# Performance work log

Hardware: AMD Instinct MI355X
Metric: run time of the kernel (lower is better)

## Reference

```python
import jax, jax.numpy as jnp
import numpy as np

# Config (DiffWave-style)
C = 64        # channels
K = 3         # kernel_size
L = 30        # num_layers
CYCLES = 3    # num_cycles
DRATE = 2     # dilation_rate
ITER = 50     # diffusion steps
ESIZE = 128   # embedding_size
EPROJ = 512   # embedding_proj
EFACT = 4.0   # embedding_factor
B, T = 4, 16384
LAYERS_PER_CYCLE = L // CYCLES
DILATIONS = [DRATE ** (i % LAYERS_PER_CYCLE) for i in range(L)]
INV_SQRT2 = 1.0 / np.sqrt(2.0).astype(np.float32)


def _embed_table():
    # [ITER, ESIZE] sinusoidal noise-schedule embedding (deterministic buffer)
    logit = jnp.linspace(0.0, 1.0, ESIZE // 2)
    exp = jnp.power(10.0, logit * EFACT)
    t = jnp.arange(1, ITER + 1, dtype=jnp.float32)
    comp = exp[None, :] * t[:, None]
    return jnp.concatenate([jnp.sin(comp), jnp.cos(comp)], axis=-1)


def _dconv(x, w, d):
    # x: [B,T,Cin], w: [K,Cin,Cout], SAME padding, dilation d -> [B,T,Cout]
    return jax.lax.conv_general_dilated(
        x, w, window_strides=(1,), padding='SAME', rhs_dilation=(d,),
        dimension_numbers=('NWC', 'WIO', 'NWC'))


def setup_inputs() -> dict:
    key = jax.random.key(0)
    ks = jax.random.split(key, 20)
    g = lambda k, shape, fan_in: (jax.random.normal(k, shape) / np.sqrt(fan_in)).astype(jnp.float32)
    return {
        'signal': jax.random.normal(ks[0], (B, T), dtype=jnp.float32),
        'timestep': jax.random.randint(ks[1], (B,), 1, ITER + 1, dtype=jnp.int32),
        'in_w': g(ks[2], (1, C), 1),
        'in_b': jnp.zeros((C,), jnp.float32),
        'pe0_w': g(ks[3], (ESIZE, EPROJ), ESIZE),
        'pe0_b': jnp.zeros((EPROJ,), jnp.float32),
        'pe1_w': g(ks[4], (EPROJ, EPROJ), EPROJ),
        'pe1_b': jnp.zeros((EPROJ,), jnp.float32),
        'blk_emb_w': g(ks[5], (L, EPROJ, C), EPROJ),
        'blk_emb_b': jnp.zeros((L, C), jnp.float32),
        'blk_conv_w': g(ks[6], (L, K, C, 2 * C), K * C),
        'blk_conv_b': jnp.zeros((L, 2 * C), jnp.float32),
        'blk_res_w': g(ks[7], (L - 1, C, C), C),
        'blk_res_b': jnp.zeros((L - 1, C), jnp.float32),
        'blk_skip_w': g(ks[8], (L, C, C), C),
        'blk_skip_b': jnp.zeros((L, C), jnp.float32),
        'out0_w': g(ks[9], (C, C), C),
        'out0_b': jnp.zeros((C,), jnp.float32),
        'out1_w': g(ks[10], (C, 1), C),
        'out1_b': jnp.zeros((1,), jnp.float32),
    }


def reference(signal, timestep, in_w, in_b, pe0_w, pe0_b, pe1_w, pe1_b,
              blk_emb_w, blk_emb_b, blk_conv_w, blk_conv_b,
              blk_res_w, blk_res_b, blk_skip_w, blk_skip_b,
              out0_w, out0_b, out1_w, out1_b):
    # input 1x1 conv + relu: [B,T] -> [B,T,C]
    x = jax.nn.relu(signal[..., None] * in_w[0][None, None, :] + in_b)
    # noise-schedule embedding [B,ESIZE] -> swish MLP -> [B,EPROJ]
    embed = _embed_table()[timestep - 1]
    embed = jax.nn.swish(embed @ pe0_w + pe0_b)
    embed = jax.nn.swish(embed @ pe1_w + pe1_b)
    skip_sum = jnp.zeros_like(x)
    for i in range(L):
        e = embed @ blk_emb_w[i] + blk_emb_b[i]           # [B,C]
        h = x + e[:, None, :]                              # [B,T,C]
        y = _dconv(h, blk_conv_w[i], DILATIONS[i]) + blk_conv_b[i]  # [B,T,2C]
        z = jnp.tanh(y[..., :C]) * jax.nn.sigmoid(y[..., C:])       # gated
        if i < L - 1:
            x = (z @ blk_res_w[i] + blk_res_b[i] + x) * INV_SQRT2
        skip_sum = skip_sum + (z @ blk_skip_w[i] + blk_skip_b[i])
    ctx = skip_sum / np.sqrt(L).astype(np.float32)
    ctx = jax.nn.relu(ctx @ out0_w + out0_b)
    out = ctx @ out1_w + out1_b                            # [B,T,1]
    return jnp.squeeze(out, axis=-1)
```

## Files before the change

kernel.cpp:

```cpp
#include <hip/hip_runtime.h>
#include <math.h>

#define TT 16384
#define BB 4
#define CC 64
#define LL 30

typedef _Float16 f16;
typedef _Float16 f16x4 __attribute__((ext_vector_type(4)));
typedef _Float16 f16x8 __attribute__((ext_vector_type(8)));
typedef float f32x4 __attribute__((ext_vector_type(4)));
typedef unsigned int u32;

#define MFMA(a, b, c) __builtin_amdgcn_mfma_f32_16x16x32_f16(a, b, c, 0, 0, 0)

__device__ __forceinline__ float fsig(float x) { return 1.0f / (1.0f + __expf(-x)); }
__device__ __forceinline__ float ftanhf(float x) { return 1.0f - 2.0f / (__expf(2.0f * x) + 1.0f); }

__device__ __forceinline__ void gl_lds16(const void* g, void* l) {
    __builtin_amdgcn_global_load_lds((const __attribute__((address_space(1))) u32*)g,
                                     (__attribute__((address_space(3))) u32*)l, 16, 0, 0);
}

__global__ void pack_weights(const float* __restrict__ conv_w, const float* __restrict__ res_w,
                             const float* __restrict__ skip_w, const float* __restrict__ out0_w,
                             f16* __restrict__ wcv, f16* __restrict__ wrs, f16* __restrict__ wsk,
                             f16* __restrict__ wo0) {
    const int total_c = LL * 6 * 8 * 64 * 8;
    const int total_r = (LL - 1) * 2 * 4 * 64 * 8;
    const int total_s = LL * 2 * 4 * 64 * 8;
    const int total_o = 2 * 4 * 64 * 8;
    const int total = total_c + total_r + total_s + total_o;
    for (int i = blockIdx.x * blockDim.x + threadIdx.x; i < total; i += gridDim.x * blockDim.x) {
        if (i < total_c) {
            int e = i & 7, lane = (i >> 3) & 63, mf = (i >> 9) & 7, rest = i >> 12;
            int ks = rest % 6, l = rest / 6;
            int cin = (ks & 1) * 32 + (lane >> 4) * 8 + e;
            int tap = ks >> 1;
            int cout = mf * 16 + (lane & 15);
            wcv[i] = (f16)conv_w[(((size_t)l * 3 + tap) * 64 + cin) * 128 + cout];
        } else if (i < total_c + total_r) {
            int j = i - total_c;
            int e = j & 7, lane = (j >> 3) & 63, mf = (j >> 9) & 3, kk = (j >> 11) & 1, l = j >> 12;
            int cin = kk * 32 + (lane >> 4) * 8 + e;
            int cout = mf * 16 + (lane & 15);
            wrs[j] = (f16)res_w[((size_t)l * 64 + cin) * 64 + cout];
        } else if (i < total_c + total_r + total_s) {
            int j = i - total_c - total_r;
            int e = j & 7, lane = (j >> 3) & 63, mf = (j >> 9) & 3, kk = (j >> 11) & 1, l = j >> 12;
            int cin = kk * 32 + (lane >> 4) * 8 + e;
            int cout = mf * 16 + (lane & 15);
            wsk[j] = (f16)skip_w[((size_t)l * 64 + cin) * 64 + cout];
        } else {
            int j = i - total_c - total_r - total_s;
            int e = j & 7, lane = (j >> 3) & 63, mf = (j >> 9) & 3, kk = (j >> 11) & 1;
            int cin = kk * 32 + (lane >> 4) * 8 + e;
            int c = mf * 16 + (lane & 15);
            wo0[j] = (f16)out0_w[cin * 64 + c];
        }
    }
}

__global__ void init_x_kernel(const float* __restrict__ signal, const float* __restrict__ in_w,
                              const float* __restrict__ in_b, f16* __restrict__ x0) {
    int i = blockIdx.x * 256 + threadIdx.x;
    int bt = i >> 3, g = i & 7;
    float s = signal[bt];
    f32x4 w0 = *(const f32x4*)&in_w[g * 8];
    f32x4 w1 = *(const f32x4*)&in_w[g * 8 + 4];
    f32x4 b0 = *(const f32x4*)&in_b[g * 8];
    f32x4 b1 = *(const f32x4*)&in_b[g * 8 + 4];
    f16x8 o;
#pragma unroll
    for (int j = 0; j < 4; ++j) {
        o[j] = (f16)fmaxf(s * w0[j] + b0[j], 0.f);
        o[4 + j] = (f16)fmaxf(s * w1[j] + b1[j], 0.f);
    }
    *(f16x8*)&x0[(size_t)bt * CC + g * 8] = o;
}

__global__ void embed_stage1(const int* __restrict__ timestep, const float* __restrict__ pe0_w,
                             const float* __restrict__ pe0_b, float* __restrict__ h1) {
    __shared__ float emb[BB * 128];
    const int tid = threadIdx.x;
    for (int i = tid; i < BB * 128; i += 256) {
        int b = i >> 7, j = i & 127, jj = j & 63;
        float logit = (jj == 63) ? 1.0f : (float)jj * (1.0f / 63.0f);
        double e10 = pow(10.0, (double)(4.0f * logit));
        float comp = (float)e10 * (float)timestep[b];
        emb[i] = (j < 64) ? (float)sin((double)comp) : (float)cos((double)comp);
    }
    __syncthreads();
    const int col = blockIdx.x * 64 + (tid & 63), b = tid >> 6;
    float s = 0.f;
    for (int j = 0; j < 128; ++j) s += emb[b * 128 + j] * pe0_w[j * 512 + col];
    s += pe0_b[col];
    h1[b * 512 + col] = s * fsig(s);
}

__global__ void embed_stage2(const float* __restrict__ h1, const float* __restrict__ pe1_w,
                             const float* __restrict__ pe1_b, float* __restrict__ embed2) {
    __shared__ float hs[BB * 512];
    const int tid = threadIdx.x;
    for (int i = tid; i < BB * 512; i += 256) hs[i] = h1[i];
    __syncthreads();
    const int col = blockIdx.x * 64 + (tid & 63), b = tid >> 6;
    float s = 0.f;
    for (int j = 0; j < 512; ++j) s += hs[b * 512 + j] * pe1_w[j * 512 + col];
    s += pe1_b[col];
    embed2[b * 512 + col] = s * fsig(s);
}

__global__ void e_kernel(const float* __restrict__ embed2, const float* __restrict__ blk_emb_w,
                         const float* __restrict__ blk_emb_b, float* __restrict__ e_out) {
    const int l = blockIdx.x, b = blockIdx.y;
    const int tid = threadIdx.x;
    __shared__ float em[512];
    __shared__ float red[256];
    for (int i = tid; i < 512; i += 256) em[i] = embed2[b * 512 + i];
    __syncthreads();
    const int c = tid & 63, part = tid >> 6;
    float s0 = 0.f, s1 = 0.f;
    for (int j = part * 128; j < part * 128 + 128; j += 2) {
        s0 += em[j] * blk_emb_w[((size_t)l * 512 + j) * 64 + c];
        s1 += em[j + 1] * blk_emb_w[((size_t)l * 512 + j + 1) * 64 + c];
    }
    red[tid] = s0 + s1;
    __syncthreads();
    if (tid < 64)
        e_out[(l * BB + b) * 64 + tid] =
            red[tid] + red[tid + 64] + red[tid + 128] + red[tid + 192] + blk_emb_b[l * 64 + tid];
}

__global__ void evec2_kernel(const float* __restrict__ e_in, const float* __restrict__ conv_w,
                             const float* __restrict__ conv_b, float* __restrict__ evec) {
    const int l = blockIdx.x, tap = blockIdx.y, b = blockIdx.z;
    const int n = threadIdx.x;
    __shared__ float es[64];
    if (n < 64) es[n] = e_in[(l * BB + b) * 64 + n];
    __syncthreads();
    const float* cw = conv_w + ((size_t)(l * 3 + tap) * 64) * 128;
    float a0 = 0.f, a1 = 0.f, a2 = 0.f, a3 = 0.f;
#pragma unroll
    for (int k = 0; k < 64; k += 4) {
        a0 += es[k] * cw[k * 128 + n];
        a1 += es[k + 1] * cw[(k + 1) * 128 + n];
        a2 += es[k + 2] * cw[(k + 2) * 128 + n];
        a3 += es[k + 3] * cw[(k + 3) * 128 + n];
    }
    float s = a0 + a1 + a2 + a3 + ((tap == 1) ? conv_b[l * 128 + n] : 0.f);
    evec[((size_t)(l * 4 + b) * 3 + tap) * 128 + n] = s;
}

__global__ void sbsum_kernel(const float* __restrict__ skip_b, float* __restrict__ sbsum) {
    int c = threadIdx.x;
    float s = 0.f;
    for (int l = 0; l < LL; ++l) s += skip_b[l * 64 + c];
    sbsum[c] = s;
}

__launch_bounds__(256)
__global__ void layer_kernel(const f16* __restrict__ xin, f16* __restrict__ xout,
                             f16* __restrict__ zg,
                             const f16* __restrict__ wcv,
                             const f16* __restrict__ wrs,
                             const float* __restrict__ evec_l,
                             const float* __restrict__ res_b,
                             const f16* __restrict__ zpage, int d) {
    __shared__ f16 xs[3 * 64 * 64];
    __shared__ f16 zs[64 * 64];
    const int tid = threadIdx.x, lane = tid & 63, w = tid >> 6;
    const int lrow = lane & 15, lk = lane >> 4;
    const int b = blockIdx.y, t0 = blockIdx.x * 64;
    const f16* xb = xin + (size_t)b * TT * CC;
    f16* zb = zg + (size_t)b * TT * CC;

#pragma unroll
    for (int j = 0; j < 6; ++j) {
        int chunk = j * 4 + w;
        int gid = chunk * 64 + lane;
        int tap = gid >> 9, row = (gid >> 3) & 63, g = gid & 7;
        int t = t0 + row + (tap - 1) * d;
        const f16* src = ((unsigned)t < TT) ? (xb + (size_t)t * CC + ((g ^ (row & 7)) << 3)) : zpage;
        gl_lds16(src, (void*)((char*)xs + chunk * 1024));
    }
    __syncthreads();

    f32x4 acc[2][4] = {};
#pragma unroll
    for (int ks = 0; ks < 6; ++ks) {
        const int tap = ks >> 1, kk = ks & 1;
        f16x8 aw0 = *(const f16x8*)&wcv[((ks * 8 + w) * 64 + lane) * 8];
        f16x8 aw1 = *(const f16x8*)&wcv[((ks * 8 + w + 4) * 64 + lane) * 8];
#pragma unroll
        for (int nfi = 0; nfi < 4; ++nfi) {
            int trow = nfi * 16 + lrow;
            int r = tap * 64 + trow;
            int g = kk * 4 + lk;
            f16x8 bx = *(const f16x8*)&xs[r * 64 + ((g ^ (r & 7)) << 3)];
            acc[0][nfi] = MFMA(aw0, bx, acc[0][nfi]);
            acc[1][nfi] = MFMA(aw1, bx, acc[1][nfi]);
        }
    }

    const float* evb = evec_l + b * 384;
    const int ca = w * 16 + lk * 4;
    const int gz = ca >> 3;
    f32x4 e0a = *(const f32x4*)&evb[ca], e1a = *(const f32x4*)&evb[128 + ca],
          e2a = *(const f32x4*)&evb[256 + ca];
    f32x4 e0b = *(const f32x4*)&evb[64 + ca], e1b = *(const f32x4*)&evb[192 + ca],
          e2b = *(const f32x4*)&evb[320 + ca];
#pragma unroll
    for (int nfi = 0; nfi < 4; ++nfi) {
        int trow = nfi * 16 + lrow;
        int t = t0 + trow;
        float m0 = (t >= d) ? 1.f : 0.f;
        float m2 = (t + d < TT) ? 1.f : 0.f;
        f16x4 zo;
#pragma unroll
        for (int r = 0; r < 4; ++r) {
            float ya = acc[0][nfi][r] + e1a[r] + m0 * e0a[r] + m2 * e2a[r];
            float yb = acc[1][nfi][r] + e1b[r] + m0 * e0b[r] + m2 * e2b[r];
            zo[r] = (f16)(ftanhf(ya) * fsig(yb));
        }
        *(f16x4*)&zs[trow * 64 + ((gz ^ (trow & 7)) << 3) + (ca & 7)] = zo;
        *(f16x4*)&zb[(size_t)(t0 + trow) * CC + ca] = zo;
    }

    if (wrs != nullptr) {
        __syncthreads();
        f32x4 accR[4] = {};
#pragma unroll
        for (int kk = 0; kk < 2; ++kk) {
            f16x8 ar_ = *(const f16x8*)&wrs[((kk * 4 + w) * 64 + lane) * 8];
#pragma unroll
            for (int nfi = 0; nfi < 4; ++nfi) {
                int trow = nfi * 16 + lrow;
                int g = kk * 4 + lk;
                f16x8 bz = *(const f16x8*)&zs[trow * 64 + ((g ^ (trow & 7)) << 3)];
                accR[nfi] = MFMA(ar_, bz, accR[nfi]);
            }
        }
        f16* xob = xout + (size_t)b * TT * CC;
        f32x4 rb4 = *(const f32x4*)&res_b[ca];
#pragma unroll
        for (int nfi = 0; nfi < 4; ++nfi) {
            int trow = nfi * 16 + lrow;
            int rr = 64 + trow;
            f16x4 xv = *(const f16x4*)&xs[rr * 64 + ((gz ^ (rr & 7)) << 3) + (ca & 7)];
            f16x4 xo;
#pragma unroll
            for (int r = 0; r < 4; ++r)
                xo[r] = (f16)((accR[nfi][r] + rb4[r] + (float)xv[r]) * 0.70710678118654752f);
            *(f16x4*)&xob[(size_t)(t0 + trow) * CC + ca] = xo;
        }
    }
}

__launch_bounds__(256)
__global__ void skip_head(const f16* __restrict__ zbuf, const f16* __restrict__ z29,
                          const f16* __restrict__ wsk, const f16* __restrict__ wo0,
                          const float* __restrict__ sbsum, const float* __restrict__ out0_b,
                          const float* __restrict__ out1_w, const float* __restrict__ out1_b,
                          float* __restrict__ out) {
    __shared__ f16 zb[4][64 * 64];
    const int tid = threadIdx.x, lane = tid & 63, w = tid >> 6;
    const int lrow = lane & 15, lk = lane >> 4;
    const int lin = blockIdx.x;
    const int lin2 = (lin & 7) * 128 + (lin >> 3);
    const int b = lin2 >> 8, tile = lin2 & 255;
    const int t0 = tile * 64;
    const int trow = w * 16 + lrow;

#define STAGE_Z(L, BUF)                                                                       \
    {                                                                                         \
        const f16* zl =                                                                       \
            (((L) < LL - 1) ? (zbuf + (size_t)(L)*BB * TT * CC) : z29) + (size_t)b * TT * CC; \
        _Pragma("unroll") for (int j = 0; j < 2; ++j) {                                       \
            int chunk = j * 4 + w;                                                            \
            int gid = chunk * 64 + lane;                                                      \
            int r = gid >> 3, g = gid & 7;                                                    \
            gl_lds16(zl + (size_t)(t0 + r) * CC + ((g ^ (r & 7)) << 3),                       \
                     (void*)((char*)zb[BUF] + chunk * 1024));                                 \
        }                                                                                     \
    }

    f32x4 accS[4] = {};
    STAGE_Z(0, 0);
    STAGE_Z(1, 1);
    for (int l = 0; l < LL; ++l) {
        if (l + 2 < LL) STAGE_Z(l + 2, (l + 2) & 3);
        if (l < LL - 2) {
            asm volatile("s_waitcnt vmcnt(4)" ::: "memory");
        } else if (l == LL - 2) {
            asm volatile("s_waitcnt vmcnt(2)" ::: "memory");
        } else {
            asm volatile("s_waitcnt vmcnt(0)" ::: "memory");
        }
        __builtin_amdgcn_s_barrier();
        __builtin_amdgcn_sched_barrier(0);
        const f16* wl = wsk + (size_t)l * 4096;
        const f16* zcur = zb[l & 3];
#pragma unroll
        for (int kk = 0; kk < 2; ++kk) {
            int g = kk * 4 + lk;
            f16x8 bz = *(const f16x8*)&zcur[trow * 64 + ((g ^ (trow & 7)) << 3)];
#pragma unroll
            for (int mf = 0; mf < 4; ++mf) {
                f16x8 as_ = *(const f16x8*)&wl[((kk * 4 + mf) * 64 + lane) * 8];
                accS[mf] = MFMA(as_, bz, accS[mf]);
            }
        }
    }

    __syncthreads();
    const float invL = 0.18257418583505537f;
#pragma unroll
    for (int mf = 0; mf < 4; ++mf) {
        const int ca = mf * 16 + lk * 4;
        f32x4 sb4 = *(const f32x4*)&sbsum[ca];
        const int g = ca >> 3;
        f16x4 sn;
#pragma unroll
        for (int r = 0; r < 4; ++r) sn[r] = (f16)((accS[mf][r] + sb4[r]) * invL);
        *(f16x4*)&zb[0][trow * 64 + ((g ^ (trow & 7)) << 3) + (ca & 7)] = sn;
    }
    __syncthreads();
    f32x4 accO[4] = {};
#pragma unroll
    for (int kk = 0; kk < 2; ++kk) {
        int g = kk * 4 + lk;
        f16x8 bz = *(const f16x8*)&zb[0][trow * 64 + ((g ^ (trow & 7)) << 3)];
#pragma unroll
        for (int mf = 0; mf < 4; ++mf) {
            f16x8 aw = *(const f16x8*)&wo0[((kk * 4 + mf) * 64 + lane) * 8];
            accO[mf] = MFMA(aw, bz, accO[mf]);
        }
    }
    float pv = 0.f;
    const float b1 = out1_b[0];
#pragma unroll
    for (int mf = 0; mf < 4; ++mf) {
        int c = mf * 16 + lk * 4;
        f32x4 b0 = *(const f32x4*)&out0_b[c];
        f32x4 w1 = *(const f32x4*)&out1_w[c];
#pragma unroll
        for (int r = 0; r < 4; ++r) pv += fmaxf(accO[mf][r] + b0[r], 0.f) * w1[r];
    }
    pv += __shfl_xor(pv, 16);
    pv += __shfl_xor(pv, 32);
    if (lane < 16) out[(size_t)b * TT + t0 + w * 16 + lane] = pv + b1;
#undef STAGE_Z
}

extern "C" void kernel_launch(void* const* d_in, const int* in_sizes, int n_in,
                              void* d_out, int out_size, void* d_ws, size_t ws_size,
                              hipStream_t stream) {
    const float* signal = (const float*)d_in[0];
    const int* timestep = (const int*)d_in[1];
    const float* in_w = (const float*)d_in[2];
    const float* in_b = (const float*)d_in[3];
    const float* pe0_w = (const float*)d_in[4];
    const float* pe0_b = (const float*)d_in[5];
    const float* pe1_w = (const float*)d_in[6];
    const float* pe1_b = (const float*)d_in[7];
    const float* blk_emb_w = (const float*)d_in[8];
    const float* blk_emb_b = (const float*)d_in[9];
    const float* blk_conv_w = (const float*)d_in[10];
    const float* blk_conv_b = (const float*)d_in[11];
    const float* blk_res_w = (const float*)d_in[12];
    const float* blk_res_b = (const float*)d_in[13];
    const float* blk_skip_w = (const float*)d_in[14];
    const float* blk_skip_b = (const float*)d_in[15];
    const float* out0_w = (const float*)d_in[16];
    const float* out0_b = (const float*)d_in[17];
    const float* out1_w = (const float*)d_in[18];
    const float* out1_b = (const float*)d_in[19];

    char* p = (char*)d_ws;
    const size_t xhsz = (size_t)BB * TT * CC * sizeof(f16);
    f16* xa = (f16*)p; p += xhsz;
    f16* xb2 = (f16*)p; p += xhsz;
    f16* wcv = (f16*)p; p += (size_t)737280 * 2;
    f16* wrs = (f16*)p; p += (size_t)118784 * 2;
    f16* wsk = (f16*)p; p += (size_t)122880 * 2;
    f16* wo0 = (f16*)p; p += (size_t)4096 * 2;
    float* h1 = (float*)p; p += 4 * 512 * sizeof(float);
    float* embed2 = (float*)p; p += 4 * 512 * sizeof(float);
    float* e_buf = (float*)p; p += (size_t)LL * BB * 64 * sizeof(float);
    float* evec = (float*)p; p += (size_t)LL * 4 * 3 * 128 * sizeof(float);
    float* sbsum = (float*)p; p += 64 * sizeof(float);
    f16* zpage = (f16*)p; p += 256;
    p = (char*)(((size_t)p + 255) & ~(size_t)255);
    f16* zbuf = (f16*)p; p += (size_t)(LL - 1) * xhsz;

    hipMemsetAsync(zpage, 0, 256, stream);
    pack_weights<<<1024, 256, 0, stream>>>(blk_conv_w, blk_res_w, blk_skip_w, out0_w,
                                           wcv, wrs, wsk, wo0);
    init_x_kernel<<<2048, 256, 0, stream>>>(signal, in_w, in_b, xa);
    embed_stage1<<<8, 256, 0, stream>>>(timestep, pe0_w, pe0_b, h1);
    embed_stage2<<<8, 256, 0, stream>>>(h1, pe1_w, pe1_b, embed2);
    e_kernel<<<dim3(LL, BB), 256, 0, stream>>>(embed2, blk_emb_w, blk_emb_b, e_buf);
    evec2_kernel<<<dim3(LL, 3, BB), 128, 0, stream>>>(e_buf, blk_conv_w, blk_conv_b, evec);
    sbsum_kernel<<<1, 64, 0, stream>>>(blk_skip_b, sbsum);

    f16* cur = xa;
    f16* nxt = xb2;
    for (int i = 0; i < LL; ++i) {
        int d = 1 << (i % 10);
        bool last = (i == LL - 1);
        f16* zg = last ? xa : (zbuf + (size_t)i * BB * TT * CC);
        layer_kernel<<<dim3(TT / 64, BB), 256, 0, stream>>>(
            cur, nxt, zg,
            wcv + (size_t)i * 24576,
            last ? nullptr : (wrs + (size_t)i * 4096),
            evec + (size_t)i * 1536,
            last ? nullptr : (blk_res_b + i * 64),
            zpage, d);
        if (!last) { f16* t = cur; cur = nxt; nxt = t; }
    }

    skip_head<<<(BB * TT) / 64, 256, 0, stream>>>(zbuf, xa, wsk, wo0, sbsum, out0_b, out1_w,
                                                  out1_b, (float*)d_out);
}
```

Before: 567.6 us.

## Fuse first four dilated layers of each cycle into one LDS-resident kernel

Adds a group kernel that runs layers with dilations 1,2,4,8 back to back on a 128-step tile plus a 32-step halo on each side, keeping the residual stream in double-buffered LDS. It replaces four separate layer launches per cycle, each of which round-trips x through global memory. The cost is redundant halo computation (192 rows computed for 128 useful), clamped reads at the halo edges, and more LDS per block, which may lower occupancy. The final z buffer pointer is adjusted so the last layer's gate output lands in the right buffer for the skip head.

```diff
diff --git a/kernel.cpp b/kernel.cpp
--- a/kernel.cpp
+++ b/kernel.cpp
@@ -160,12 +160,122 @@
 }
 
 __launch_bounds__(256)
+__global__ void group4_kernel(const f16* __restrict__ xin, f16* __restrict__ xout,
+                              f16* __restrict__ zg_base,
+                              const f16* __restrict__ wcv_g,
+                              const f16* __restrict__ wrs_g,
+                              const float* __restrict__ evec_g,
+                              const float* __restrict__ res_b_g,
+                              const f16* __restrict__ zpage) {
+    __shared__ f16 lds[2 * 192 * 64];
+    const int tid = threadIdx.x, lane = tid & 63, w = tid >> 6;
+    const int lrow = lane & 15, lk = lane >> 4;
+    const int b = blockIdx.y, t0 = blockIdx.x * 128;
+    const int ca = w * 16 + lk * 4, gz = ca >> 3;
+    const f16* xbg = xin + (size_t)b * TT * CC;
+
+#pragma unroll
+    for (int j = 0; j < 6; ++j) {
+        int chunk = j * 4 + w;
+        int gid = chunk * 64 + lane;
+        int r = gid >> 3, g = gid & 7;
+        int t = t0 - 32 + r;
+        const f16* src = ((unsigned)t < TT) ? (xbg + (size_t)t * CC + ((g ^ (r & 7)) << 3)) : zpage;
+        gl_lds16(src, (void*)((char*)lds + chunk * 1024));
+    }
+    __syncthreads();
+
+#pragma unroll
+    for (int li = 0; li < 4; ++li) {
+        const int d = 1 << li;
+        f16* xc = lds + (li & 1) * (192 * 64);
+        f16* xn = lds + ((li & 1) ^ 1) * (192 * 64);
+        const f16* wcv_l = wcv_g + (size_t)li * 24576;
+        const f16* wrs_l = wrs_g + (size_t)li * 4096;
+        f16* zb_g = zg_base + (size_t)li * ((size_t)BB * TT * CC) + (size_t)b * TT * CC;
+        const float* evb = evec_g + li * 1536 + b * 384;
+
+        f32x4 acc0[12] = {}, acc1[12] = {};
+#pragma unroll
+        for (int ks = 0; ks < 6; ++ks) {
+            const int tap = ks >> 1, kk = ks & 1;
+            f16x8 aw0 = *(const f16x8*)&wcv_l[((ks * 8 + w) * 64 + lane) * 8];
+            f16x8 aw1 = *(const f16x8*)&wcv_l[((ks * 8 + w + 4) * 64 + lane) * 8];
+#pragma unroll
+            for (int nt = 0; nt < 12; ++nt) {
+                int rr = nt * 16 + lrow + (tap - 1) * d;
+                rr = (rr < 0) ? 0 : (rr > 191 ? 191 : rr);
+                int g = kk * 4 + lk;
+                f16x8 bx = *(const f16x8*)&xc[rr * 64 + ((g ^ (rr & 7)) << 3)];
+                acc0[nt] = MFMA(aw0, bx, acc0[nt]);
+                acc1[nt] = MFMA(aw1, bx, acc1[nt]);
+            }
+        }
+        __syncthreads();
+
+        f32x4 e0a = *(const f32x4*)&evb[ca], e1a = *(const f32x4*)&evb[128 + ca],
+              e2a = *(const f32x4*)&evb[256 + ca];
+        f32x4 e0b = *(const f32x4*)&evb[64 + ca], e1b = *(const f32x4*)&evb[192 + ca],
+              e2b = *(const f32x4*)&evb[320 + ca];
+        f16x4 xv[12];
+#pragma unroll
+        for (int nt = 0; nt < 12; ++nt) {
+            int lr = nt * 16 + lrow;
+            int t = t0 - 32 + lr;
+            xv[nt] = *(const f16x4*)&xc[lr * 64 + ((gz ^ (lr & 7)) << 3) + (ca & 7)];
+            float m0 = (t >= d) ? 1.f : 0.f;
+            float m2 = (t + d < TT) ? 1.f : 0.f;
+            f16x4 zo;
+#pragma unroll
+            for (int r = 0; r < 4; ++r) {
+                float ya = acc0[nt][r] + e1a[r] + m0 * e0a[r] + m2 * e2a[r];
+                float yb = acc1[nt][r] + e1b[r] + m0 * e0b[r] + m2 * e2b[r];
+                zo[r] = (f16)(ftanhf(ya) * fsig(yb));
+            }
+            *(f16x4*)&xc[lr * 64 + ((gz ^ (lr & 7)) << 3) + (ca & 7)] = zo;
+            if (nt >= 2 && nt < 10) *(f16x4*)&zb_g[(size_t)t * CC + ca] = zo;
+        }
+        __syncthreads();
+
+        f32x4 accR[12] = {};
+#pragma unroll
+        for (int kk = 0; kk < 2; ++kk) {
+            f16x8 ar = *(const f16x8*)&wrs_l[((kk * 4 + w) * 64 + lane) * 8];
+#pragma unroll
+            for (int nt = 0; nt < 12; ++nt) {
+                int lr = nt * 16 + lrow;
+                int g = kk * 4 + lk;
+                f16x8 bz = *(const f16x8*)&xc[lr * 64 + ((g ^ (lr & 7)) << 3)];
+                accR[nt] = MFMA(ar, bz, accR[nt]);
+            }
+        }
+        f32x4 rb4 = *(const f32x4*)&res_b_g[li * 64 + ca];
+        f16* xog = xout + (size_t)b * TT * CC;
+#pragma unroll
+        for (int nt = 0; nt < 12; ++nt) {
+            int lr = nt * 16 + lrow;
+            int t = t0 - 32 + lr;
+            bool tin = ((unsigned)t < TT);
+            f16x4 xo;
+#pragma unroll
+            for (int r = 0; r < 4; ++r)
+                xo[r] = tin ? (f16)((accR[nt][r] + rb4[r] + (float)xv[nt][r]) * 0.70710678118654752f)
+                            : (f16)0;
+            if (li < 3) {
+                *(f16x4*)&xn[lr * 64 + ((gz ^ (lr & 7)) << 3) + (ca & 7)] = xo;
+            } else if (nt >= 2 && nt < 10) {
+                *(f16x4*)&xog[(size_t)t * CC + ca] = xo;
+            }
+        }
+        __syncthreads();
+    }
+}
+
+__launch_bounds__(256)
 __global__ void layer_kernel(const f16* __restrict__ xin, f16* __restrict__ xout,
                              f16* __restrict__ zg,
-                             const f16* __restrict__ wcv,
-                             const f16* __restrict__ wrs,
-                             const float* __restrict__ evec_l,
-                             const float* __restrict__ res_b,
+                             const f16* __restrict__ wcv, const f16* __restrict__ wrs,
+                             const float* __restrict__ evec_l, const float* __restrict__ res_b,
                              const f16* __restrict__ zpage, int d) {
     __shared__ f16 xs[3 * 64 * 64];
     __shared__ f16 zs[64 * 64];
@@ -379,6 +489,7 @@
 
     char* p = (char*)d_ws;
     const size_t xhsz = (size_t)BB * TT * CC * sizeof(f16);
+    const size_t BTC = (size_t)BB * TT * CC;
     f16* xa = (f16*)p; p += xhsz;
     f16* xb2 = (f16*)p; p += xhsz;
     f16* wcv = (f16*)p; p += (size_t)737280 * 2;
@@ -406,20 +517,28 @@
 
     f16* cur = xa;
     f16* nxt = xb2;
-    for (int i = 0; i < LL; ++i) {
-        int d = 1 << (i % 10);
-        bool last = (i == LL - 1);
-        f16* zg = last ? xa : (zbuf + (size_t)i * BB * TT * CC);
-        layer_kernel<<<dim3(TT / 64, BB), 256, 0, stream>>>(
-            cur, nxt, zg,
-            wcv + (size_t)i * 24576,
-            last ? nullptr : (wrs + (size_t)i * 4096),
-            evec + (size_t)i * 1536,
-            last ? nullptr : (blk_res_b + i * 64),
-            zpage, d);
-        if (!last) { f16* t = cur; cur = nxt; nxt = t; }
-    }
-
-    skip_head<<<(BB * TT) / 64, 256, 0, stream>>>(zbuf, xa, wsk, wo0, sbsum, out0_b, out1_w,
+    f16* z29 = xa;
+    for (int i = 0; i < LL;) {
+        if (i % 10 == 0) {
+            group4_kernel<<<dim3(TT / 128, BB), 256, 0, stream>>>(
+                cur, nxt, zbuf + (size_t)i * BTC, wcv + (size_t)i * 24576,
+                wrs + (size_t)i * 4096, evec + (size_t)i * 1536, blk_res_b + i * 64, zpage);
+            f16* t = cur; cur = nxt; nxt = t;
+            i += 4;
+        } else {
+            int d = 1 << (i % 10);
+            bool last = (i == LL - 1);
+            f16* zg = last ? nxt : (zbuf + (size_t)i * BTC);
+            if (last) z29 = nxt;
+            layer_kernel<<<dim3(TT / 64, BB), 256, 0, stream>>>(
+                cur, nxt, zg, wcv + (size_t)i * 24576,
+                last ? nullptr : (wrs + (size_t)i * 4096), evec + (size_t)i * 1536,
+                last ? nullptr : (blk_res_b + i * 64), zpage, d);
+            if (!last) { f16* t = cur; cur = nxt; nxt = t; }
+            i += 1;
+        }
+    }
+
+    skip_head<<<(BB * TT) / 64, 256, 0, stream>>>(zbuf, z29, wsk, wo0, sbsum, out0_b, out1_w,
                                                   out1_b, (float*)d_out);
 }
```

Result: slower. 1.034 ms (+82.2%).

## Split skip-head layer reduction across waves with register loads and LDS reduction

Applied to the files above, without the earlier changes.

The skip_head kernel used to have all four waves work through the 30 layers in sequence. It staged each layer's z tile into LDS and placed a block barrier between layers. Now each wave owns every fourth layer and loads z straight into registers with double buffering. It accumulates the full 64x64 tile, and the four partial sums are then reduced through a padded LDS buffer before the output MLP. The aim is to remove the 30 per-layer barriers and the LDS staging traffic, at the cost of more accumulator registers, a serialized four-phase reduction, and uncoalesced per-lane global loads.

```diff
diff --git a/kernel.cpp b/kernel.cpp
--- a/kernel.cpp
+++ b/kernel.cpp
@@ -162,10 +162,8 @@
 __launch_bounds__(256)
 __global__ void layer_kernel(const f16* __restrict__ xin, f16* __restrict__ xout,
                              f16* __restrict__ zg,
-                             const f16* __restrict__ wcv,
-                             const f16* __restrict__ wrs,
-                             const float* __restrict__ evec_l,
-                             const float* __restrict__ res_b,
+                             const f16* __restrict__ wcv, const f16* __restrict__ wrs,
+                             const float* __restrict__ evec_l, const float* __restrict__ res_b,
                              const f16* __restrict__ zpage, int d) {
     __shared__ f16 xs[3 * 64 * 64];
     __shared__ f16 zs[64 * 64];
@@ -263,74 +261,88 @@
                           const float* __restrict__ sbsum, const float* __restrict__ out0_b,
                           const float* __restrict__ out1_w, const float* __restrict__ out1_b,
                           float* __restrict__ out) {
-    __shared__ f16 zb[4][64 * 64];
+    __shared__ float red[64 * 65];
     const int tid = threadIdx.x, lane = tid & 63, w = tid >> 6;
     const int lrow = lane & 15, lk = lane >> 4;
     const int lin = blockIdx.x;
     const int lin2 = (lin & 7) * 128 + (lin >> 3);
     const int b = lin2 >> 8, tile = lin2 & 255;
     const int t0 = tile * 64;
+
+#define ZL(L) ((((L) < LL - 1) ? (zbuf + (size_t)(L) * BB * TT * CC) : z29) + \
+               ((size_t)b * TT + t0) * CC)
+#define ZLOAD(DST, ZP)                                                           \
+    _Pragma("unroll") for (int nt = 0; nt < 4; ++nt) _Pragma("unroll")           \
+        for (int kk = 0; kk < 2; ++kk) {                                         \
+        DST[nt * 2 + kk] =                                                       \
+            *(const f16x8*)((ZP) + ((size_t)(nt * 16 + lrow)) * CC + kk * 32 + lk * 8); \
+    }
+
+    f32x4 accS[4][4] = {};
+    f16x8 zr[2][8];
+    {
+        const f16* zp0 = ZL(w);
+        ZLOAD(zr[0], zp0);
+    }
+#pragma unroll
+    for (int li = 0; li < 8; ++li) {
+        const int l = w + li * 4;
+        if (l < LL) {
+            if (l + 4 < LL) {
+                const f16* zpn = ZL(l + 4);
+                ZLOAD(zr[(li + 1) & 1], zpn);
+            }
+            const f16* wl = wsk + (size_t)l * 4096;
+#pragma unroll
+            for (int kk = 0; kk < 2; ++kk) {
+#pragma unroll
+                for (int mf = 0; mf < 4; ++mf) {
+                    f16x8 as_ = *(const f16x8*)&wl[((kk * 4 + mf) * 64 + lane) * 8];
+#pragma unroll
+                    for (int nt = 0; nt < 4; ++nt)
+                        accS[mf][nt] = MFMA(as_, zr[li & 1][nt * 2 + kk], accS[mf][nt]);
+                }
+            }
+        }
+    }
+#undef ZLOAD
+#undef ZL
+
+    __syncthreads();
+#pragma unroll
+    for (int ph = 0; ph < 4; ++ph) {
+        if (w == ph) {
+#pragma unroll
+            for (int mf = 0; mf < 4; ++mf) {
+#pragma unroll
+                for (int nt = 0; nt < 4; ++nt) {
+                    int row = nt * 16 + lrow;
+                    int base = row * 65 + mf * 16 + lk * 4;
+#pragma unroll
+                    for (int r = 0; r < 4; ++r) {
+                        if (ph == 0) red[base + r] = accS[mf][nt][r];
+                        else red[base + r] += accS[mf][nt][r];
+                    }
+                }
+            }
+        }
+        __syncthreads();
+    }
+
+    const float invL = 0.18257418583505537f;
     const int trow = w * 16 + lrow;
-
-#define STAGE_Z(L, BUF)                                                                       \
-    {                                                                                         \
-        const f16* zl =                                                                       \
-            (((L) < LL - 1) ? (zbuf + (size_t)(L)*BB * TT * CC) : z29) + (size_t)b * TT * CC; \
-        _Pragma("unroll") for (int j = 0; j < 2; ++j) {                                       \
-            int chunk = j * 4 + w;                                                            \
-            int gid = chunk * 64 + lane;                                                      \
-            int r = gid >> 3, g = gid & 7;                                                    \
-            gl_lds16(zl + (size_t)(t0 + r) * CC + ((g ^ (r & 7)) << 3),                       \
-                     (void*)((char*)zb[BUF] + chunk * 1024));                                 \
-        }                                                                                     \
-    }
-
-    f32x4 accS[4] = {};
-    STAGE_Z(0, 0);
-    STAGE_Z(1, 1);
-    for (int l = 0; l < LL; ++l) {
-        if (l + 2 < LL) STAGE_Z(l + 2, (l + 2) & 3);
-        if (l < LL - 2) {
-            asm volatile("s_waitcnt vmcnt(4)" ::: "memory");
-        } else if (l == LL - 2) {
-            asm volatile("s_waitcnt vmcnt(2)" ::: "memory");
-        } else {
-            asm volatile("s_waitcnt vmcnt(0)" ::: "memory");
-        }
-        __builtin_amdgcn_s_barrier();
-        __builtin_amdgcn_sched_barrier(0);
-        const f16* wl = wsk + (size_t)l * 4096;
-        const f16* zcur = zb[l & 3];
-#pragma unroll
-        for (int kk = 0; kk < 2; ++kk) {
-            int g = kk * 4 + lk;
-            f16x8 bz = *(const f16x8*)&zcur[trow * 64 + ((g ^ (trow & 7)) << 3)];
-#pragma unroll
-            for (int mf = 0; mf < 4; ++mf) {
-                f16x8 as_ = *(const f16x8*)&wl[((kk * 4 + mf) * 64 + lane) * 8];
-                accS[mf] = MFMA(as_, bz, accS[mf]);
-            }
-        }
-    }
-
-    __syncthreads();
-    const float invL = 0.18257418583505537f;
-#pragma unroll
-    for (int mf = 0; mf < 4; ++mf) {
-        const int ca = mf * 16 + lk * 4;
-        f32x4 sb4 = *(const f32x4*)&sbsum[ca];
-        const int g = ca >> 3;
-        f16x4 sn;
-#pragma unroll
-        for (int r = 0; r < 4; ++r) sn[r] = (f16)((accS[mf][r] + sb4[r]) * invL);
-        *(f16x4*)&zb[0][trow * 64 + ((g ^ (trow & 7)) << 3) + (ca & 7)] = sn;
-    }
-    __syncthreads();
     f32x4 accO[4] = {};
 #pragma unroll
     for (int kk = 0; kk < 2; ++kk) {
-        int g = kk * 4 + lk;
-        f16x8 bz = *(const f16x8*)&zb[0][trow * 64 + ((g ^ (trow & 7)) << 3)];
+        const int ch0 = kk * 32 + lk * 8;
+        f32x4 sb0 = *(const f32x4*)&sbsum[ch0];
+        f32x4 sb1 = *(const f32x4*)&sbsum[ch0 + 4];
+        f16x8 bz;
+#pragma unroll
+        for (int j = 0; j < 4; ++j) {
+            bz[j] = (f16)((red[trow * 65 + ch0 + j] + sb0[j]) * invL);
+            bz[4 + j] = (f16)((red[trow * 65 + ch0 + 4 + j] + sb1[j]) * invL);
+        }
 #pragma unroll
         for (int mf = 0; mf < 4; ++mf) {
             f16x8 aw = *(const f16x8*)&wo0[((kk * 4 + mf) * 64 + lane) * 8];
@@ -350,7 +362,6 @@
     pv += __shfl_xor(pv, 16);
     pv += __shfl_xor(pv, 32);
     if (lane < 16) out[(size_t)b * TT + t0 + w * 16 + lane] = pv + b1;
-#undef STAGE_Z
 }
 
 extern "C" void kernel_launch(void* const* d_in, const int* in_sizes, int n_in,
@@ -379,6 +390,7 @@
 
     char* p = (char*)d_ws;
     const size_t xhsz = (size_t)BB * TT * CC * sizeof(f16);
+    const size_t BTC = (size_t)BB * TT * CC;
     f16* xa = (f16*)p; p += xhsz;
     f16* xb2 = (f16*)p; p += xhsz;
     f16* wcv = (f16*)p; p += (size_t)737280 * 2;
@@ -406,20 +418,19 @@
 
     f16* cur = xa;
     f16* nxt = xb2;
+    f16* z29 = xa;
     for (int i = 0; i < LL; ++i) {
         int d = 1 << (i % 10);
         bool last = (i == LL - 1);
-        f16* zg = last ? xa : (zbuf + (size_t)i * BB * TT * CC);
+        f16* zg = last ? nxt : (zbuf + (size_t)i * BTC);
+        if (last) z29 = nxt;
         layer_kernel<<<dim3(TT / 64, BB), 256, 0, stream>>>(
-            cur, nxt, zg,
-            wcv + (size_t)i * 24576,
-            last ? nullptr : (wrs + (size_t)i * 4096),
-            evec + (size_t)i * 1536,
-            last ? nullptr : (blk_res_b + i * 64),
-            zpage, d);
+            cur, nxt, zg, wcv + (size_t)i * 24576,
+            last ? nullptr : (wrs + (size_t)i * 4096), evec + (size_t)i * 1536,
+            last ? nullptr : (blk_res_b + i * 64), zpage, d);
         if (!last) { f16* t = cur; cur = nxt; nxt = t; }
     }
 
-    skip_head<<<(BB * TT) / 64, 256, 0, stream>>>(zbuf, xa, wsk, wo0, sbsum, out0_b, out1_w,
+    skip_head<<<(BB * TT) / 64, 256, 0, stream>>>(zbuf, z29, wsk, wo0, sbsum, out0_b, out1_w,
                                                   out1_b, (float*)d_out);
 }
```

Measured after the change: 565.7 us. Within noise of the previous version (-0.3%).

## Share overlapping dilated-conv tap rows in LDS and shrink skip_head buffering

Applied to the files above, without the earlier changes.

The layer kernel now stages only the distinct time rows the three taps need (64 + 2*min(d,64) rows) into dynamic shared memory. For small dilations the overlapping taps reuse the same rows instead of loading three separate 64-row windows, which cuts global loads and LDS footprint and may allow higher occupancy. skip_head moves from a four-buffer, depth-two prefetch with manual waitcnt to a two-buffer, depth-one prefetch with __syncthreads, and remaps waves so each wave owns an output-channel slice across all time rows. The last layer's z output now goes to the spare ping-pong buffer. The shallower prefetch may expose more load latency in skip_head.

```diff
diff --git a/kernel.cpp b/kernel.cpp
--- a/kernel.cpp
+++ b/kernel.cpp
@@ -162,26 +162,26 @@
 __launch_bounds__(256)
 __global__ void layer_kernel(const f16* __restrict__ xin, f16* __restrict__ xout,
                              f16* __restrict__ zg,
-                             const f16* __restrict__ wcv,
-                             const f16* __restrict__ wrs,
-                             const float* __restrict__ evec_l,
-                             const float* __restrict__ res_b,
+                             const f16* __restrict__ wcv, const f16* __restrict__ wrs,
+                             const float* __restrict__ evec_l, const float* __restrict__ res_b,
                              const f16* __restrict__ zpage, int d) {
-    __shared__ f16 xs[3 * 64 * 64];
-    __shared__ f16 zs[64 * 64];
+    extern __shared__ f16 lds[];
     const int tid = threadIdx.x, lane = tid & 63, w = tid >> 6;
     const int lrow = lane & 15, lk = lane >> 4;
     const int b = blockIdx.y, t0 = blockIdx.x * 64;
+    const int stride = (d < 64) ? d : 64;
+    const int R8 = (64 + 2 * stride + 7) & ~7;
+    f16* xs = lds;
+    f16* zs = lds + R8 * 64;
     const f16* xb = xin + (size_t)b * TT * CC;
     f16* zb = zg + (size_t)b * TT * CC;
 
-#pragma unroll
-    for (int j = 0; j < 6; ++j) {
-        int chunk = j * 4 + w;
+    const int NCH = R8 >> 3;
+    for (int chunk = w; chunk < NCH; chunk += 4) {
         int gid = chunk * 64 + lane;
-        int tap = gid >> 9, row = (gid >> 3) & 63, g = gid & 7;
-        int t = t0 + row + (tap - 1) * d;
-        const f16* src = ((unsigned)t < TT) ? (xb + (size_t)t * CC + ((g ^ (row & 7)) << 3)) : zpage;
+        int r = gid >> 3, g = gid & 7;
+        int t = t0 - d + r + ((d > 64) ? ((r >> 6) * (d - 64)) : 0);
+        const f16* src = ((unsigned)t < TT) ? (xb + (size_t)t * CC + ((g ^ (r & 7)) << 3)) : zpage;
         gl_lds16(src, (void*)((char*)xs + chunk * 1024));
     }
     __syncthreads();
@@ -194,8 +194,7 @@
         f16x8 aw1 = *(const f16x8*)&wcv[((ks * 8 + w + 4) * 64 + lane) * 8];
 #pragma unroll
         for (int nfi = 0; nfi < 4; ++nfi) {
-            int trow = nfi * 16 + lrow;
-            int r = tap * 64 + trow;
+            int r = nfi * 16 + lrow + tap * stride;
             int g = kk * 4 + lk;
             f16x8 bx = *(const f16x8*)&xs[r * 64 + ((g ^ (r & 7)) << 3)];
             acc[0][nfi] = MFMA(aw0, bx, acc[0][nfi]);
@@ -246,7 +245,7 @@
 #pragma unroll
         for (int nfi = 0; nfi < 4; ++nfi) {
             int trow = nfi * 16 + lrow;
-            int rr = 64 + trow;
+            int rr = stride + trow;
             f16x4 xv = *(const f16x4*)&xs[rr * 64 + ((gz ^ (rr & 7)) << 3) + (ca & 7)];
             f16x4 xo;
 #pragma unroll
@@ -263,14 +262,13 @@
                           const float* __restrict__ sbsum, const float* __restrict__ out0_b,
                           const float* __restrict__ out1_w, const float* __restrict__ out1_b,
                           float* __restrict__ out) {
-    __shared__ f16 zb[4][64 * 64];
+    __shared__ f16 zb[2][64 * 64];
     const int tid = threadIdx.x, lane = tid & 63, w = tid >> 6;
     const int lrow = lane & 15, lk = lane >> 4;
     const int lin = blockIdx.x;
     const int lin2 = (lin & 7) * 128 + (lin >> 3);
     const int b = lin2 >> 8, tile = lin2 & 255;
     const int t0 = tile * 64;
-    const int trow = w * 16 + lrow;
 
 #define STAGE_Z(L, BUF)                                                                       \
     {                                                                                         \
@@ -287,45 +285,40 @@
 
     f32x4 accS[4] = {};
     STAGE_Z(0, 0);
-    STAGE_Z(1, 1);
     for (int l = 0; l < LL; ++l) {
-        if (l + 2 < LL) STAGE_Z(l + 2, (l + 2) & 3);
-        if (l < LL - 2) {
-            asm volatile("s_waitcnt vmcnt(4)" ::: "memory");
-        } else if (l == LL - 2) {
-            asm volatile("s_waitcnt vmcnt(2)" ::: "memory");
-        } else {
-            asm volatile("s_waitcnt vmcnt(0)" ::: "memory");
-        }
-        __builtin_amdgcn_s_barrier();
-        __builtin_amdgcn_sched_barrier(0);
+        __syncthreads();
+        if (l + 1 < LL) STAGE_Z(l + 1, (l + 1) & 1);
         const f16* wl = wsk + (size_t)l * 4096;
-        const f16* zcur = zb[l & 3];
+        const f16* zcur = zb[l & 1];
 #pragma unroll
         for (int kk = 0; kk < 2; ++kk) {
-            int g = kk * 4 + lk;
-            f16x8 bz = *(const f16x8*)&zcur[trow * 64 + ((g ^ (trow & 7)) << 3)];
-#pragma unroll
-            for (int mf = 0; mf < 4; ++mf) {
-                f16x8 as_ = *(const f16x8*)&wl[((kk * 4 + mf) * 64 + lane) * 8];
-                accS[mf] = MFMA(as_, bz, accS[mf]);
+            f16x8 as_ = *(const f16x8*)&wl[((kk * 4 + w) * 64 + lane) * 8];
+#pragma unroll
+            for (int nt = 0; nt < 4; ++nt) {
+                int trow = nt * 16 + lrow;
+                int g = kk * 4 + lk;
+                f16x8 bz = *(const f16x8*)&zcur[trow * 64 + ((g ^ (trow & 7)) << 3)];
+                accS[nt] = MFMA(as_, bz, accS[nt]);
             }
         }
     }
 
     __syncthreads();
     const float invL = 0.18257418583505537f;
-#pragma unroll
-    for (int mf = 0; mf < 4; ++mf) {
-        const int ca = mf * 16 + lk * 4;
-        f32x4 sb4 = *(const f32x4*)&sbsum[ca];
-        const int g = ca >> 3;
+    const int cb = w * 16 + lk * 4;
+    const int gz = cb >> 3;
+    f32x4 sb4 = *(const f32x4*)&sbsum[cb];
+#pragma unroll
+    for (int nt = 0; nt < 4; ++nt) {
+        int row = nt * 16 + lrow;
         f16x4 sn;
 #pragma unroll
-        for (int r = 0; r < 4; ++r) sn[r] = (f16)((accS[mf][r] + sb4[r]) * invL);
-        *(f16x4*)&zb[0][trow * 64 + ((g ^ (trow & 7)) << 3) + (ca & 7)] = sn;
-    }
-    __syncthreads();
+        for (int r = 0; r < 4; ++r) sn[r] = (f16)((accS[nt][r] + sb4[r]) * invL);
+        *(f16x4*)&zb[0][row * 64 + ((gz ^ (row & 7)) << 3) + (cb & 7)] = sn;
+    }
+    __syncthreads();
+
+    const int trow = w * 16 + lrow;
     f32x4 accO[4] = {};
 #pragma unroll
     for (int kk = 0; kk < 2; ++kk) {
@@ -379,6 +372,7 @@
 
     char* p = (char*)d_ws;
     const size_t xhsz = (size_t)BB * TT * CC * sizeof(f16);
+    const size_t BTC = (size_t)BB * TT * CC;
     f16* xa = (f16*)p; p += xhsz;
     f16* xb2 = (f16*)p; p += xhsz;
     f16* wcv = (f16*)p; p += (size_t)737280 * 2;
@@ -406,20 +400,22 @@
 
     f16* cur = xa;
     f16* nxt = xb2;
+    f16* z29 = xa;
     for (int i = 0; i < LL; ++i) {
         int d = 1 << (i % 10);
         bool last = (i == LL - 1);
-        f16* zg = last ? xa : (zbuf + (size_t)i * BB * TT * CC);
-        layer_kernel<<<dim3(TT / 64, BB), 256, 0, stream>>>(
-            cur, nxt, zg,
-            wcv + (size_t)i * 24576,
-            last ? nullptr : (wrs + (size_t)i * 4096),
-            evec + (size_t)i * 1536,
-            last ? nullptr : (blk_res_b + i * 64),
-            zpage, d);
+        f16* zg = last ? nxt : (zbuf + (size_t)i * BTC);
+        if (last) z29 = nxt;
+        int stride = (d < 64) ? d : 64;
+        int R8 = (64 + 2 * stride + 7) & ~7;
+        size_t smem = (size_t)(R8 * 64 + 64 * 64) * sizeof(f16);
+        layer_kernel<<<dim3(TT / 64, BB), 256, smem, stream>>>(
+            cur, nxt, zg, wcv + (size_t)i * 24576,
+            last ? nullptr : (wrs + (size_t)i * 4096), evec + (size_t)i * 1536,
+            last ? nullptr : (blk_res_b + i * 64), zpage, d);
         if (!last) { f16* t = cur; cur = nxt; nxt = t; }
     }
 
-    skip_head<<<(BB * TT) / 64, 256, 0, stream>>>(zbuf, xa, wsk, wo0, sbsum, out0_b, out1_w,
+    skip_head<<<(BB * TT) / 64, 256, 0, stream>>>(zbuf, z29, wsk, wo0, sbsum, out0_b, out1_w,
                                                   out1_b, (float*)d_out);
 }
```

Result: faster. 541.3 us (-4.6%).
